# Kernel optimization log

Hardware: AMD Instinct MI355X
Metric: run time of the kernel (lower is better)

The kernel has to match this reference:

```python
import jax, jax.numpy as jnp
import numpy as np

B, N, T, H, KV = 8, 32, 1, 128, 4096
SCALE = H ** -0.5


def setup_inputs() -> dict:
    key = jax.random.key(0)
    kq, kk, kv_ = jax.random.split(key, 3)
    q = jax.random.normal(kq, (B, N, T, H), dtype=jnp.float32)
    k = jax.random.normal(kk, (B, N, KV, H), dtype=jnp.float32)
    v = jax.random.normal(kv_, (B, N, KV, H), dtype=jnp.float32)
    mask = jnp.zeros((B, 1, 1, KV), dtype=jnp.float32)
    return {"q": q, "k": k, "v": v, "mask": mask}


def reference(q, k, v, mask):
    # q: [B,N,T,H], k/v: [B,N,KV,H], mask: [B,1,1,KV]
    qs = q * jnp.asarray(SCALE, q.dtype)
    scores = jnp.einsum("bnth,bnkh->bntk", qs, k) + mask  # [B,N,T,KV]
    attn = jax.nn.softmax(scores, axis=-1)
    out = jnp.einsum("bntk,bnkh->bnth", attn, v)  # [B,N,T,H]
    return out
```

## Files before the change

### kernel.cpp

```cpp
#include <hip/hip_runtime.h>

#define BATCH 8
#define NHEADS 32
#define HDIM 128
#define KVLEN 4096
#define SCALE 0.08838834764831843f

constexpr int THREADS = 1024;
constexpr int GROUPS  = THREADS / 32;
constexpr int H4      = HDIM / 4;

__global__ __launch_bounds__(THREADS) void attn_decode_kernel(
    const float* __restrict__ q, const float* __restrict__ k,
    const float* __restrict__ v, const float* __restrict__ mask,
    float* __restrict__ out)
{
    __shared__ float s_scores[KVLEN];
    __shared__ float s_red[THREADS];
    __shared__ float s_part[GROUPS * HDIM];

    const int bn  = blockIdx.x;
    const int b   = bn / NHEADS;
    const int tid = threadIdx.x;
    const int grp = tid >> 5;
    const int l32 = tid & 31;

    const float4* __restrict__ K4 = (const float4*)k;
    const float4* __restrict__ V4 = (const float4*)v;
    const float4* __restrict__ Q4 = (const float4*)q;

    const size_t base4 = (size_t)bn * KVLEN * H4;
    const float4 q4 = Q4[(size_t)bn * H4 + l32];
    const float* __restrict__ mrow = mask + (size_t)b * KVLEN;

    float mloc = -3.4e38f;
    for (int kk = grp; kk < KVLEN; kk += GROUPS) {
        const float4 kv4 = K4[base4 + (size_t)kk * H4 + l32];
        float p = q4.x * kv4.x + q4.y * kv4.y + q4.z * kv4.z + q4.w * kv4.w;
        p += __shfl_xor(p, 16);
        p += __shfl_xor(p, 8);
        p += __shfl_xor(p, 4);
        p += __shfl_xor(p, 2);
        p += __shfl_xor(p, 1);
        const float s = p * SCALE + mrow[kk];
        mloc = fmaxf(mloc, s);
        if (l32 == 0) s_scores[kk] = s;
    }
    s_red[tid] = mloc;
    __syncthreads();
    for (int s = THREADS / 2; s > 0; s >>= 1) {
        if (tid < s) s_red[tid] = fmaxf(s_red[tid], s_red[tid + s]);
        __syncthreads();
    }
    const float m = s_red[0];
    __syncthreads();

    float sloc = 0.f;
    for (int kk = tid; kk < KVLEN; kk += THREADS) {
        const float p = __expf(s_scores[kk] - m);
        s_scores[kk] = p;
        sloc += p;
    }
    s_red[tid] = sloc;
    __syncthreads();
    for (int s = THREADS / 2; s > 0; s >>= 1) {
        if (tid < s) s_red[tid] += s_red[tid + s];
        __syncthreads();
    }
    const float inv = 1.0f / s_red[0];

    float a0 = 0.f, a1 = 0.f, a2 = 0.f, a3 = 0.f;
    for (int kk = grp; kk < KVLEN; kk += GROUPS) {
        const float p = s_scores[kk];
        const float4 v4 = V4[base4 + (size_t)kk * H4 + l32];
        a0 += p * v4.x; a1 += p * v4.y; a2 += p * v4.z; a3 += p * v4.w;
    }
    float* pp = s_part + grp * HDIM + l32 * 4;
    pp[0] = a0; pp[1] = a1; pp[2] = a2; pp[3] = a3;
    __syncthreads();
    if (tid < HDIM) {
        float acc = 0.f;
        #pragma unroll
        for (int g = 0; g < GROUPS; ++g) acc += s_part[g * HDIM + tid];
        out[(size_t)bn * HDIM + tid] = acc * inv;
    }
}

extern "C" void kernel_launch(void* const* d_in, const int* in_sizes, int n_in,
                              void* d_out, int out_size, void* d_ws, size_t ws_size,
                              hipStream_t stream) {
    const float* q    = (const float*)d_in[0];
    const float* k    = (const float*)d_in[1];
    const float* v    = (const float*)d_in[2];
    const float* mask = (const float*)d_in[3];
    float* out = (float*)d_out;

    attn_decode_kernel<<<BATCH * NHEADS, THREADS, 0, stream>>>(q, k, v, mask, out);
}
```

Baseline: 202.3 us.

## Fuse score, softmax and value passes into single online-softmax loop

Replaces the three-pass decode attention (scores, block reductions for max and sum, then V accumulation) with a single streaming loop that loads K and V together and maintains per-group running max, sum and accumulators. Per-group partial results are merged once at the end with rescaling. This removes the log-depth shared-memory reductions and their many barriers and puts more global loads in flight per iteration. In exchange it adds two exponentials per key per lane and a loop-carried dependency on the running max.

```diff
diff --git a/kernel.cpp b/kernel.cpp
--- a/kernel.cpp
+++ b/kernel.cpp
@@ -9,15 +9,16 @@
 constexpr int THREADS = 1024;
 constexpr int GROUPS  = THREADS / 32;
 constexpr int H4      = HDIM / 4;
+constexpr int ITERS   = KVLEN / GROUPS;
 
-__global__ __launch_bounds__(THREADS) void attn_decode_kernel(
+__global__ __launch_bounds__(THREADS) void attn_decode_online(
     const float* __restrict__ q, const float* __restrict__ k,
     const float* __restrict__ v, const float* __restrict__ mask,
     float* __restrict__ out)
 {
-    __shared__ float s_scores[KVLEN];
-    __shared__ float s_red[THREADS];
-    __shared__ float s_part[GROUPS * HDIM];
+    __shared__ float s_m[GROUPS];
+    __shared__ float s_l[GROUPS];
+    __shared__ float s_acc[GROUPS * HDIM];
 
     const int bn  = blockIdx.x;
     const int b   = bn / NHEADS;
@@ -33,56 +34,52 @@
     const float4 q4 = Q4[(size_t)bn * H4 + l32];
     const float* __restrict__ mrow = mask + (size_t)b * KVLEN;
 
-    float mloc = -3.4e38f;
-    for (int kk = grp; kk < KVLEN; kk += GROUPS) {
-        const float4 kv4 = K4[base4 + (size_t)kk * H4 + l32];
+    float m = -3.0e38f, l = 0.f;
+    float a0 = 0.f, a1 = 0.f, a2 = 0.f, a3 = 0.f;
+
+    #pragma unroll 2
+    for (int i = 0; i < ITERS; ++i) {
+        const int kk = grp + i * GROUPS;
+        const size_t roff = base4 + (size_t)kk * H4 + l32;
+        const float4 kv4 = K4[roff];
+        const float4 vv4 = V4[roff];
+
         float p = q4.x * kv4.x + q4.y * kv4.y + q4.z * kv4.z + q4.w * kv4.w;
         p += __shfl_xor(p, 16);
         p += __shfl_xor(p, 8);
         p += __shfl_xor(p, 4);
         p += __shfl_xor(p, 2);
         p += __shfl_xor(p, 1);
-        const float s = p * SCALE + mrow[kk];
-        mloc = fmaxf(mloc, s);
-        if (l32 == 0) s_scores[kk] = s;
+
+        const float s    = p * SCALE + mrow[kk];
+        const float mnew = fmaxf(m, s);
+        const float c    = __expf(m - mnew);
+        const float pe   = __expf(s - mnew);
+        l  = l * c + pe;
+        a0 = a0 * c + pe * vv4.x;
+        a1 = a1 * c + pe * vv4.y;
+        a2 = a2 * c + pe * vv4.z;
+        a3 = a3 * c + pe * vv4.w;
+        m  = mnew;
     }
-    s_red[tid] = mloc;
-    __syncthreads();
-    for (int s = THREADS / 2; s > 0; s >>= 1) {
-        if (tid < s) s_red[tid] = fmaxf(s_red[tid], s_red[tid + s]);
-        __syncthreads();
-    }
-    const float m = s_red[0];
+
+    float* pp = s_acc + grp * HDIM + l32 * 4;
+    pp[0] = a0; pp[1] = a1; pp[2] = a2; pp[3] = a3;
+    if (l32 == 0) { s_m[grp] = m; s_l[grp] = l; }
     __syncthreads();
 
-    float sloc = 0.f;
-    for (int kk = tid; kk < KVLEN; kk += THREADS) {
-        const float p = __expf(s_scores[kk] - m);
-        s_scores[kk] = p;
-        sloc += p;
-    }
-    s_red[tid] = sloc;
-    __syncthreads();
-    for (int s = THREADS / 2; s > 0; s >>= 1) {
-        if (tid < s) s_red[tid] += s_red[tid + s];
-        __syncthreads();
-    }
-    const float inv = 1.0f / s_red[0];
-
-    float a0 = 0.f, a1 = 0.f, a2 = 0.f, a3 = 0.f;
-    for (int kk = grp; kk < KVLEN; kk += GROUPS) {
-        const float p = s_scores[kk];
-        const float4 v4 = V4[base4 + (size_t)kk * H4 + l32];
-        a0 += p * v4.x; a1 += p * v4.y; a2 += p * v4.z; a3 += p * v4.w;
-    }
-    float* pp = s_part + grp * HDIM + l32 * 4;
-    pp[0] = a0; pp[1] = a1; pp[2] = a2; pp[3] = a3;
-    __syncthreads();
     if (tid < HDIM) {
-        float acc = 0.f;
+        float M = -3.0e38f;
         #pragma unroll
-        for (int g = 0; g < GROUPS; ++g) acc += s_part[g * HDIM + tid];
-        out[(size_t)bn * HDIM + tid] = acc * inv;
+        for (int g = 0; g < GROUPS; ++g) M = fmaxf(M, s_m[g]);
+        float denom = 0.f, acc = 0.f;
+        #pragma unroll
+        for (int g = 0; g < GROUPS; ++g) {
+            const float w = __expf(s_m[g] - M);
+            denom += s_l[g] * w;
+            acc   += s_acc[g * HDIM + tid] * w;
+        }
+        out[(size_t)bn * HDIM + tid] = acc / denom;
     }
 }
 
@@ -95,5 +92,5 @@
     const float* mask = (const float*)d_in[3];
     float* out = (float*)d_out;
 
-    attn_decode_kernel<<<BATCH * NHEADS, THREADS, 0, stream>>>(q, k, v, mask, out);
+    attn_decode_online<<<BATCH * NHEADS, THREADS, 0, stream>>>(q, k, v, mask, out);
 }
```

Result: faster. 185.5 us (-8.3%).
